# Optimization experiments

Hardware: AMD Instinct MI355X
Metric: run time of the kernel (lower is better)

The kernel has to match this reference:

```python
import jax, jax.numpy as jnp
import numpy as np


def dwconv1d(u, w, b):
    # u: (B, C, L), w: (C, 1, 3) depthwise, padding=1 -> same length
    out = jax.lax.conv_general_dilated(
        u, w, window_strides=(1,), padding=[(1, 1)],
        dimension_numbers=('NCH', 'OIH', 'NCH'),
        feature_group_count=u.shape[1])
    return out + b[None, :, None]


def selective_scan(u, delta, A, Bm, Cm, D, delta_bias):
    # u, delta: (B, KD, L); A: (KD, N); Bm, Cm: (B, K, N, L); D, delta_bias: (KD,)
    Bsz, KD, L = u.shape
    K, N = Bm.shape[1], Bm.shape[2]
    Dg = KD // K
    delta = jax.nn.softplus(delta + delta_bias[None, :, None])
    Bexp = jnp.repeat(Bm, Dg, axis=1)  # (B, KD, N, L)
    Cexp = jnp.repeat(Cm, Dg, axis=1)
    dA = jnp.exp(delta[:, :, None, :] * A[None, :, :, None])        # (B, KD, N, L)
    dBu = delta[:, :, None, :] * Bexp * u[:, :, None, :]            # (B, KD, N, L)

    def step(h, inp):
        a, bu, c = inp
        h = a * h + bu
        return h, jnp.sum(h * c, axis=-1)

    a_t = jnp.moveaxis(dA, -1, 0)
    bu_t = jnp.moveaxis(dBu, -1, 0)
    c_t = jnp.moveaxis(Cexp, -1, 0)
    _, ys = jax.lax.scan(step, jnp.zeros((Bsz, KD, N), u.dtype), (a_t, bu_t, c_t))
    return jnp.moveaxis(ys, 0, -1) + D[None, :, None] * u           # (B, KD, L)


def setup_inputs():
    key = jax.random.key(0)
    ks = jax.random.split(key, 8)
    d_inner, d_state, dt_rank, K = 192, 16, 6, 1
    bincounts = np.array([4096, 3000, 3500, 2500])
    total = int(bincounts.sum())
    max_bin = int(bincounts.max())
    starts = np.concatenate([[0], np.cumsum(bincounts)[:-1]])
    # compute_padding: wrap-around padded gather indices per cloud
    padded_idx = np.concatenate([np.arange(max_bin) % bc + st for bc, st in zip(bincounts, starts)])
    # crop-back indices into the (B*max_bin) padded layout
    valid_idx = np.concatenate([i * max_bin + np.arange(bc) for i, bc in enumerate(bincounts)])
    order = np.stack([np.random.RandomState(0).permutation(total)])
    inverse = np.argsort(order, axis=1)
    x = jax.random.normal(ks[0], (d_inner, total), jnp.float32)
    x_proj_weight = jax.random.normal(ks[1], (K, dt_rank + 2 * d_state, d_inner), jnp.float32) * 0.05
    dt_projs_weight = jax.random.normal(ks[2], (K, d_inner, dt_rank), jnp.float32) * 0.1
    dt_projs_bias = jax.random.normal(ks[3], (K, d_inner), jnp.float32) * 0.1
    A_logs = jnp.log(jnp.tile(jnp.arange(1, d_state + 1, dtype=jnp.float32), (K * d_inner, 1)))
    Ds = jnp.ones((K * d_inner,), jnp.float32)
    conv_w = jax.random.normal(ks[4], (K * d_inner, 1, 3), jnp.float32) * 0.2
    conv_b = jnp.zeros((K * d_inner,), jnp.float32)
    ln_gamma = jnp.ones((d_inner,), jnp.float32)
    ln_beta = jnp.zeros((d_inner,), jnp.float32)
    return {
        'x': x, 'x_proj_weight': x_proj_weight, 'dt_projs_weight': dt_projs_weight,
        'dt_projs_bias': dt_projs_bias, 'A_logs': A_logs, 'Ds': Ds,
        'conv_w': conv_w, 'conv_b': conv_b, 'ln_gamma': ln_gamma, 'ln_beta': ln_beta,
        'order': jnp.asarray(order, jnp.int32), 'inverse': jnp.asarray(inverse, jnp.int32),
        'padded_idx': jnp.asarray(padded_idx, jnp.int32),
        'valid_idx': jnp.asarray(valid_idx, jnp.int32), 'max_bin': max_bin,
    }


def reference(x, x_proj_weight, dt_projs_weight, dt_projs_bias, A_logs, Ds,
              conv_w, conv_b, ln_gamma, ln_beta,
              order, inverse, padded_idx, valid_idx, max_bin):
    K, Dch, R = dt_projs_weight.shape
    N = A_logs.shape[1]
    BM = padded_idx.shape[0]
    Bsz = BM // max_bin
    # multi-directional gather with offset padding: x[:, order[k]][:, padded_idx]
    idx = jnp.take(order, padded_idx, axis=1)                       # (K, B*max_bin)
    xs = jnp.take(x, idx, axis=1)                                   # (Dch, K, B*max_bin)
    xs = xs.transpose(1, 0, 2).reshape(K, Dch, Bsz, max_bin).transpose(2, 0, 1, 3)  # (B,K,D,L)
    x_dbl = jnp.einsum('bkdl,kcd->bkcl', xs, x_proj_weight)         # (B,K,R+2N,L)
    dts, Bs, Cs = jnp.split(x_dbl, [R, R + N], axis=2)
    dts = jnp.einsum('bkrl,kdr->bkdl', dts, dt_projs_weight)
    u = xs.reshape(Bsz, K * Dch, max_bin)
    delta = dts.reshape(Bsz, K * Dch, max_bin)
    A = -jnp.exp(A_logs)
    u = dwconv1d(u, conv_w, conv_b)  # conv1d applied after x_dbl/dts, before scan
    ys = selective_scan(u, delta, A, Bs, Cs, Ds, dt_projs_bias.reshape(-1))  # (B, K*Dch, L)
    # crop padding per cloud and concat along points
    ys = ys.reshape(Bsz, K, Dch, max_bin).transpose(1, 2, 0, 3).reshape(K, Dch, BM)
    ys = jnp.take(ys, valid_idx, axis=2)                            # (K, Dch, total)
    # K == 1, y_proj_weight is None -> scatter back through inverse permutation
    y = jnp.take(ys[0], inverse[0], axis=1)                         # (Dch, total)
    y = y.T                                                         # (total, Dch)
    mu = jnp.mean(y, axis=-1, keepdims=True)
    var = jnp.var(y, axis=-1, keepdims=True)
    y = (y - mu) / jnp.sqrt(var + 1e-5) * ln_gamma + ln_beta        # LayerNorm(d_inner)
    return y
```

## Files before the change

kernel.cpp:

```cpp
#include <hip/hip_runtime.h>
#include <math.h>

#define DINNER 192
#define NST    16
#define RNK    6
#define LSEQ   4096
#define BSZ    4
#define TOTAL  13096
#define BMPAD  16384
#define CL     32
#define MAXC   128
#define NSTATE 3072
#define NB32   410

#define BC_OF(b)  ((b)==0?4096:(b)==1?3000:(b)==2?3500:2500)
#define QST_OF(b) ((b)==0?0:(b)==1?4096:(b)==2?7096:10596)
#define NCB_OF(b) ((b)==0?128:(b)==1?94:(b)==2?110:79)

__device__ float  g_xs[(size_t)TOTAL * DINNER];
__device__ float  g_BC[(size_t)TOTAL * 32];
__device__ float  g_dt[(size_t)TOTAL * 8];
__device__ float2 g_PQ[(size_t)BSZ * MAXC * NSTATE];
__device__ float  g_hin[(size_t)BSZ * MAXC * NSTATE];

__global__ __launch_bounds__(256) void kA(
    const float* __restrict__ x,
    const float* __restrict__ W,
    const int*   __restrict__ inverse)
{
    const int blk = blockIdx.x;
    const int t = threadIdx.x;
    const bool isG = (blk >= NB32);
    const int P0 = (isG ? blk - NB32 : blk) * 32;
    const int npts = min(32, TOTAL - P0);

    __shared__ float sx[32 * 193];
    __shared__ float sW[38 * DINNER];
    __shared__ int   sg[32];

    if (t < 32) sg[t] = (t < npts) ? inverse[P0 + t] : 0;
    for (int idx = t; idx < 32 * DINNER; idx += 256) {
        int j = idx & 31, d = idx >> 5;
        sx[j * 193 + d] = (j < npts) ? x[(size_t)d * TOTAL + P0 + j] : 0.f;
    }
    if (isG)
        for (int idx = t; idx < 38 * DINNER; idx += 256) sW[idx] = W[idx];
    __syncthreads();

    if (!isG) {
        for (int idx = t; idx < npts * 48; idx += 256) {
            int j = idx / 48, q = idx - j * 48;
            const float* sp = &sx[j * 193 + q * 4];
            float4 v = {sp[0], sp[1], sp[2], sp[3]};
            *(float4*)&g_xs[(size_t)sg[j] * DINNER + q * 4] = v;
        }
    } else {
        const int j = t & 31, cw = t >> 5;
        float acc[5] = {0.f, 0.f, 0.f, 0.f, 0.f};
        for (int dt0 = 0; dt0 < DINNER; dt0 += 16) {
            float xr[16];
            #pragma unroll
            for (int q = 0; q < 16; ++q) xr[q] = sx[j * 193 + dt0 + q];
            #pragma unroll
            for (int k = 0; k < 5; ++k) {
                const int c = cw + 8 * k;
                if (c < RNK + 2 * NST) {
                    const float4* wr = (const float4*)&sW[c * DINNER + dt0];
                    float4 w0 = wr[0], w1 = wr[1], w2 = wr[2], w3 = wr[3];
                    float a = acc[k];
                    a += xr[0]*w0.x + xr[1]*w0.y + xr[2]*w0.z + xr[3]*w0.w;
                    a += xr[4]*w1.x + xr[5]*w1.y + xr[6]*w1.z + xr[7]*w1.w;
                    a += xr[8]*w2.x + xr[9]*w2.y + xr[10]*w2.z + xr[11]*w2.w;
                    a += xr[12]*w3.x + xr[13]*w3.y + xr[14]*w3.z + xr[15]*w3.w;
                    acc[k] = a;
                }
            }
        }
        if (j < npts) {
            const int g = sg[j];
            #pragma unroll
            for (int k = 0; k < 5; ++k) {
                const int c = cw + 8 * k;
                if (c < RNK)                g_dt[(size_t)g * 8 + c] = acc[k];
                else if (c < RNK + 2 * NST) g_BC[(size_t)g * 32 + (c - RNK)] = acc[k];
            }
        }
    }
}

__device__ __forceinline__ float xpad(int pos, int bc, int qst, int d) {
    if (pos < 0 || pos >= LSEQ) return 0.f;
    if (pos >= bc) pos -= bc;
    return g_xs[(size_t)(qst + pos) * DINNER + d];
}

__global__ __launch_bounds__(192) void k2_scan1(
    const float* __restrict__ A_logs,
    const float* __restrict__ conv_w,
    const float* __restrict__ conv_b,
    const float* __restrict__ dtW,
    const float* __restrict__ dtB)
{
    const int blk = blockIdx.x;
    const int b = blk >> 7;
    const int chunk = blk & (MAXC - 1);
    const int bc = BC_OF(b), qst = QST_OF(b), ncb = NCB_OF(b);
    if (chunk >= ncb) return;
    const int l0 = chunk * CL;
    const int steps = min(CL, bc - l0);
    const int t = threadIdx.x;

    __shared__ float sxr[(CL + 2) * DINNER];
    __shared__ float sB[CL * NST];
    __shared__ float sdt[CL * 8];

    for (int k = 0; k < steps + 2; ++k)
        sxr[k * DINNER + t] = xpad(l0 - 1 + k, bc, qst, t);
    for (int idx = t; idx < steps * NST; idx += 192) {
        int i = idx >> 4, n = idx & 15;
        sB[idx] = g_BC[(size_t)(qst + l0 + i) * 32 + n];
    }
    for (int idx = t; idx < steps * 8; idx += 192)
        sdt[idx] = g_dt[(size_t)(qst + l0) * 8 + idx];
    __syncthreads();

    float Av[16];
    {
        const float4* A4 = (const float4*)(A_logs + t * NST);
        #pragma unroll
        for (int q = 0; q < 4; ++q) {
            float4 v = A4[q];
            Av[q*4+0] = -__expf(v.x); Av[q*4+1] = -__expf(v.y);
            Av[q*4+2] = -__expf(v.z); Av[q*4+3] = -__expf(v.w);
        }
    }
    const float Av0 = Av[0];
    bool fast = true;
    #pragma unroll
    for (int n = 0; n < 16; ++n)
        fast = fast && (fabsf(Av[n] - (float)(n + 1) * Av0) <= 1e-4f * (float)(n + 1));

    float wdt[RNK];
    #pragma unroll
    for (int r = 0; r < RNK; ++r) wdt[r] = dtW[t * RNK + r];
    const float bdel = dtB[t];
    const float cw0 = conv_w[t*3+0], cw1 = conv_w[t*3+1], cw2 = conv_w[t*3+2];
    const float cb = conv_b[t];

    float h[16];
    #pragma unroll
    for (int n = 0; n < 16; ++n) h[n] = 0.f;
    float delsum = 0.f;
    float xm = sxr[t], xc = sxr[DINNER + t];

    for (int i = 0; i < steps; ++i) {
        float xp = sxr[(i + 2) * DINNER + t];
        float u = fmaf(cw0, xm, fmaf(cw1, xc, fmaf(cw2, xp, cb)));
        float da = bdel;
        #pragma unroll
        for (int r = 0; r < RNK; ++r) da = fmaf(wdt[r], sdt[i * 8 + r], da);
        float del = (da > 20.f) ? da : log1pf(__expf(da));
        float du = del * u;
        delsum += del;
        const float4* b4 = (const float4*)&sB[i * NST];
        float4 B0 = b4[0], B1 = b4[1], B2 = b4[2], B3 = b4[3];
        const float Bv[16] = {B0.x,B0.y,B0.z,B0.w, B1.x,B1.y,B1.z,B1.w,
                              B2.x,B2.y,B2.z,B2.w, B3.x,B3.y,B3.z,B3.w};
        if (fast) {
            float e = __expf(del * Av0);
            float a = e;
            #pragma unroll
            for (int n = 0; n < 16; ++n) { h[n] = fmaf(a, h[n], Bv[n] * du); a *= e; }
        } else {
            #pragma unroll
            for (int n = 0; n < 16; ++n) {
                float a = __expf(del * Av[n]);
                h[n] = fmaf(a, h[n], Bv[n] * du);
            }
        }
        xm = xc; xc = xp;
    }

    float4* o4 = (float4*)(g_PQ + (size_t)(b * MAXC + chunk) * NSTATE + t * 16);
    #pragma unroll
    for (int k = 0; k < 8; ++k) {
        float P0v = __expf(Av[2*k]   * delsum);
        float P1v = __expf(Av[2*k+1] * delsum);
        o4[k] = make_float4(P0v, h[2*k], P1v, h[2*k+1]);
    }
}

__global__ __launch_bounds__(256) void k3_comb()
{
    const int b = blockIdx.x / 48;
    const int s0 = (blockIdx.x % 48) * 64;
    const int ncb = NCB_OF(b);
    const int t = threadIdx.x;
    __shared__ float2 spq[MAXC * 64];

    for (int idx = t; idx < ncb * 64; idx += 256) {
        int c = idx >> 6, j = idx & 63;
        spq[idx] = g_PQ[(size_t)(b * MAXC + c) * NSTATE + s0 + j];
    }
    __syncthreads();
    if (t < 64) {
        float h = 0.f;
        for (int c = 0; c < ncb; ++c) {
            g_hin[(size_t)(b * MAXC + c) * NSTATE + s0 + t] = h;
            float2 v = spq[c * 64 + t];
            h = fmaf(v.x, h, v.y);
        }
    }
}

__global__ __launch_bounds__(192) void k4_scan2(
    const float* __restrict__ A_logs,
    const float* __restrict__ conv_w,
    const float* __restrict__ conv_b,
    const float* __restrict__ dtW,
    const float* __restrict__ dtB,
    const float* __restrict__ Ds,
    const int*   __restrict__ order,
    const float* __restrict__ gamma,
    const float* __restrict__ beta,
    float* __restrict__ out)
{
    const int blk = blockIdx.x;
    const int b = blk >> 7;
    const int chunk = blk & (MAXC - 1);
    const int bc = BC_OF(b), qst = QST_OF(b), ncb = NCB_OF(b);
    if (chunk >= ncb) return;
    const int l0 = chunk * CL;
    const int steps = min(CL, bc - l0);
    const int t = threadIdx.x;

    __shared__ float sxr[(CL + 2) * DINNER];
    __shared__ float sBC[CL * 32];
    __shared__ float sdt[CL * 8];
    __shared__ float sy[CL * DINNER];

    for (int k = 0; k < steps + 2; ++k)
        sxr[k * DINNER + t] = xpad(l0 - 1 + k, bc, qst, t);
    {
        const size_t base = (size_t)(qst + l0) * 32;
        for (int idx = t; idx < steps * 32; idx += 192) sBC[idx] = g_BC[base + idx];
    }
    for (int idx = t; idx < steps * 8; idx += 192)
        sdt[idx] = g_dt[(size_t)(qst + l0) * 8 + idx];
    __syncthreads();

    float Av[16];
    {
        const float4* A4 = (const float4*)(A_logs + t * NST);
        #pragma unroll
        for (int q = 0; q < 4; ++q) {
            float4 v = A4[q];
            Av[q*4+0] = -__expf(v.x); Av[q*4+1] = -__expf(v.y);
            Av[q*4+2] = -__expf(v.z); Av[q*4+3] = -__expf(v.w);
        }
    }
    const float Av0 = Av[0];
    bool fast = true;
    #pragma unroll
    for (int n = 0; n < 16; ++n)
        fast = fast && (fabsf(Av[n] - (float)(n + 1) * Av0) <= 1e-4f * (float)(n + 1));

    float wdt[RNK];
    #pragma unroll
    for (int r = 0; r < RNK; ++r) wdt[r] = dtW[t * RNK + r];
    const float bdel = dtB[t];
    const float cw0 = conv_w[t*3+0], cw1 = conv_w[t*3+1], cw2 = conv_w[t*3+2];
    const float cb = conv_b[t];
    const float Dd = Ds[t];

    float h[16];
    {
        const float4* h4 = (const float4*)(g_hin + (size_t)(b * MAXC + chunk) * NSTATE + t * 16);
        #pragma unroll
        for (int q = 0; q < 4; ++q) *(float4*)&h[q * 4] = h4[q];
    }
    float xm = sxr[t], xc = sxr[DINNER + t];

    for (int i = 0; i < steps; ++i) {
        float xp = sxr[(i + 2) * DINNER + t];
        float u = fmaf(cw0, xm, fmaf(cw1, xc, fmaf(cw2, xp, cb)));
        float da = bdel;
        #pragma unroll
        for (int r = 0; r < RNK; ++r) da = fmaf(wdt[r], sdt[i * 8 + r], da);
        float del = (da > 20.f) ? da : log1pf(__expf(da));
        float du = del * u;
        const float4* b4 = (const float4*)&sBC[i * 32];
        float4 B0 = b4[0], B1 = b4[1], B2 = b4[2], B3 = b4[3];
        float4 C0 = b4[4], C1 = b4[5], C2 = b4[6], C3 = b4[7];
        const float Bv[16] = {B0.x,B0.y,B0.z,B0.w, B1.x,B1.y,B1.z,B1.w,
                              B2.x,B2.y,B2.z,B2.w, B3.x,B3.y,B3.z,B3.w};
        const float Cv[16] = {C0.x,C0.y,C0.z,C0.w, C1.x,C1.y,C1.z,C1.w,
                              C2.x,C2.y,C2.z,C2.w, C3.x,C3.y,C3.z,C3.w};
        float y = Dd * u;
        if (fast) {
            float e = __expf(del * Av0);
            float a = e;
            #pragma unroll
            for (int n = 0; n < 16; ++n) {
                h[n] = fmaf(a, h[n], Bv[n] * du);
                y = fmaf(h[n], Cv[n], y);
                a *= e;
            }
        } else {
            #pragma unroll
            for (int n = 0; n < 16; ++n) {
                float a = __expf(del * Av[n]);
                h[n] = fmaf(a, h[n], Bv[n] * du);
                y = fmaf(h[n], Cv[n], y);
            }
        }
        sy[i * DINNER + t] = y;
        xm = xc; xc = xp;
    }
    __syncthreads();

    const int wv = t >> 6;
    const int lane = t & 63;
    for (int i = wv; i < steps; i += 3) {
        const float v0 = sy[i * DINNER + lane];
        const float v1 = sy[i * DINNER + 64 + lane];
        const float v2 = sy[i * DINNER + 128 + lane];
        float s  = v0 + v1 + v2;
        float s2 = v0 * v0 + v1 * v1 + v2 * v2;
        #pragma unroll
        for (int off = 1; off < 64; off <<= 1) {
            s  += __shfl_xor(s,  off);
            s2 += __shfl_xor(s2, off);
        }
        const float mu   = s / (float)DINNER;
        const float var  = s2 / (float)DINNER - mu * mu;
        const float rstd = rsqrtf(var + 1e-5f);
        const int p = order[qst + l0 + i];
        float* orow = out + (size_t)p * DINNER;
        orow[lane]       = (v0 - mu) * rstd * gamma[lane]       + beta[lane];
        orow[lane + 64]  = (v1 - mu) * rstd * gamma[lane + 64]  + beta[lane + 64];
        orow[lane + 128] = (v2 - mu) * rstd * gamma[lane + 128] + beta[lane + 128];
    }
}

extern "C" void kernel_launch(void* const* d_in, const int* in_sizes, int n_in,
                              void* d_out, int out_size, void* d_ws, size_t ws_size,
                              hipStream_t stream) {
    const float* x       = (const float*)d_in[0];
    const float* W       = (const float*)d_in[1];
    const float* dtW     = (const float*)d_in[2];
    const float* dtB     = (const float*)d_in[3];
    const float* A_logs  = (const float*)d_in[4];
    const float* Ds      = (const float*)d_in[5];
    const float* conv_w  = (const float*)d_in[6];
    const float* conv_b  = (const float*)d_in[7];
    const float* gamma   = (const float*)d_in[8];
    const float* beta    = (const float*)d_in[9];
    const int*   order   = (const int*)d_in[10];
    const int*   inverse = (const int*)d_in[11];
    float* outp = (float*)d_out;

    if (in_sizes[0] != TOTAL * DINNER || in_sizes[12] != BMPAD) return;

    kA<<<2 * NB32, 256, 0, stream>>>(x, W, inverse);
    k2_scan1<<<BSZ * MAXC, 192, 0, stream>>>(A_logs, conv_w, conv_b, dtW, dtB);
    k3_comb<<<192, 256, 0, stream>>>();
    k4_scan2<<<BSZ * MAXC, 192, 0, stream>>>(A_logs, conv_w, conv_b, dtW, dtB,
                                             Ds, order, gamma, beta, outp);
}
```

Before: 203.1 us.

## Fuse all four stages into one cooperative kernel with grid syncs

Replaces the four-kernel pipeline (projection, chunk scan, chunk combine, final scan plus LayerNorm) with a single cooperative kernel of 512 blocks that separates the stages with grid.sync. Each chunk block's shared-memory inputs (x window, B/C, dt) are loaded once and reused by both scan passes. The chunk combine is spread over all blocks, one state chain per thread, instead of running on 192 blocks. The kernel also detects when A's rows form an arithmetic sequence and computes the per-state decays with one exp and repeated multiplies. This removes launch gaps and repeated global loads, at the cost of grid-wide barriers and the requirement that all 512 blocks be co-resident, with a fallback to the old path.

New measurement: 527.0 us. +159.5%, slower.

```diff
diff --git a/kernel.cpp b/kernel.cpp
--- a/kernel.cpp
+++ b/kernel.cpp
@@ -1,5 +1,8 @@
 #include <hip/hip_runtime.h>
+#include <hip/hip_cooperative_groups.h>
 #include <math.h>
+
+namespace cg = cooperative_groups;
 
 #define DINNER 192
 #define NST    16
@@ -11,6 +14,7 @@
 #define CL     32
 #define MAXC   128
 #define NSTATE 3072
+#define NCHAIN 12288
 #define NB32   410
 
 #define BC_OF(b)  ((b)==0?4096:(b)==1?3000:(b)==2?3500:2500)
@@ -23,10 +27,278 @@
 __device__ float2 g_PQ[(size_t)BSZ * MAXC * NSTATE];
 __device__ float  g_hin[(size_t)BSZ * MAXC * NSTATE];
 
-__global__ __launch_bounds__(256) void kA(
+__device__ __forceinline__ float xpad(int pos, int bc, int qst, int d) {
+    if (pos < 0 || pos >= LSEQ) return 0.f;
+    if (pos >= bc) pos -= bc;
+    return g_xs[(size_t)(qst + pos) * DINNER + d];
+}
+
+__global__ __launch_bounds__(192, 1) void k_fused(
     const float* __restrict__ x,
     const float* __restrict__ W,
-    const int*   __restrict__ inverse)
+    const int*   __restrict__ inverse,
+    const float* __restrict__ A_logs,
+    const float* __restrict__ conv_w,
+    const float* __restrict__ conv_b,
+    const float* __restrict__ dtW,
+    const float* __restrict__ dtB,
+    const float* __restrict__ Ds,
+    const int*   __restrict__ order,
+    const float* __restrict__ gamma,
+    const float* __restrict__ beta,
+    float* __restrict__ out)
+{
+    cg::grid_group grid = cg::this_grid();
+    const int blk = blockIdx.x;
+    const int t = threadIdx.x;
+
+    __shared__ __align__(16) union {
+        struct { float sx[32 * 193]; float sW[38 * DINNER]; int sg[32]; } p1;
+        struct { float sxr[(CL + 2) * DINNER]; float sy[CL * DINNER];
+                 float sBC[CL * 32]; float sdt[CL * 8]; } p2;
+    } u;
+
+    if (blk < NB32) {
+        const int P0 = blk * 32;
+        const int npts = min(32, TOTAL - P0);
+        if (t < 32) u.p1.sg[t] = (t < npts) ? inverse[P0 + t] : 0;
+        for (int idx = t; idx < 32 * DINNER; idx += 192) {
+            int j = idx & 31, d = idx >> 5;
+            u.p1.sx[j * 193 + d] = (j < npts) ? x[(size_t)d * TOTAL + P0 + j] : 0.f;
+        }
+        for (int idx = t; idx < 38 * DINNER; idx += 192) u.p1.sW[idx] = W[idx];
+        __syncthreads();
+
+        for (int idx = t; idx < npts * 48; idx += 192) {
+            int j = idx / 48, q = idx - j * 48;
+            const float* sp = &u.p1.sx[j * 193 + q * 4];
+            float4 v = {sp[0], sp[1], sp[2], sp[3]};
+            *(float4*)&g_xs[(size_t)u.p1.sg[j] * DINNER + q * 4] = v;
+        }
+        const int j = t & 31, cw = t >> 5;
+        float acc[7] = {0.f, 0.f, 0.f, 0.f, 0.f, 0.f, 0.f};
+        for (int dt0 = 0; dt0 < DINNER; dt0 += 16) {
+            float xr[16];
+            #pragma unroll
+            for (int q = 0; q < 16; ++q) xr[q] = u.p1.sx[j * 193 + dt0 + q];
+            #pragma unroll
+            for (int k = 0; k < 7; ++k) {
+                const int c = cw + 6 * k;
+                if (c < RNK + 2 * NST) {
+                    const float4* wr = (const float4*)&u.p1.sW[c * DINNER + dt0];
+                    float4 w0 = wr[0], w1 = wr[1], w2 = wr[2], w3 = wr[3];
+                    float a = acc[k];
+                    a += xr[0]*w0.x + xr[1]*w0.y + xr[2]*w0.z + xr[3]*w0.w;
+                    a += xr[4]*w1.x + xr[5]*w1.y + xr[6]*w1.z + xr[7]*w1.w;
+                    a += xr[8]*w2.x + xr[9]*w2.y + xr[10]*w2.z + xr[11]*w2.w;
+                    a += xr[12]*w3.x + xr[13]*w3.y + xr[14]*w3.z + xr[15]*w3.w;
+                    acc[k] = a;
+                }
+            }
+        }
+        if (j < npts) {
+            const int g = u.p1.sg[j];
+            #pragma unroll
+            for (int k = 0; k < 7; ++k) {
+                const int c = cw + 6 * k;
+                if (c < RNK)                g_dt[(size_t)g * 8 + c] = acc[k];
+                else if (c < RNK + 2*NST)   g_BC[(size_t)g * 32 + (c - RNK)] = acc[k];
+            }
+        }
+    }
+    __threadfence();
+    grid.sync();
+
+    const int b = blk >> 7;
+    const int chunk = blk & (MAXC - 1);
+    const int bc = BC_OF(b), qst = QST_OF(b), ncb = NCB_OF(b);
+    const bool act = (chunk < ncb);
+    const int l0 = chunk * CL;
+    const int steps = act ? min(CL, bc - l0) : 0;
+
+    float Av[16];
+    {
+        const float4* A4 = (const float4*)(A_logs + t * NST);
+        #pragma unroll
+        for (int q = 0; q < 4; ++q) {
+            float4 v = A4[q];
+            Av[q*4+0] = -__expf(v.x); Av[q*4+1] = -__expf(v.y);
+            Av[q*4+2] = -__expf(v.z); Av[q*4+3] = -__expf(v.w);
+        }
+    }
+    const float Av0 = Av[0];
+    bool fast = true;
+    #pragma unroll
+    for (int n = 0; n < 16; ++n)
+        fast = fast && (fabsf(Av[n] - (float)(n + 1) * Av0) <= 1e-4f * (float)(n + 1));
+
+    float wdt[RNK];
+    #pragma unroll
+    for (int r = 0; r < RNK; ++r) wdt[r] = dtW[t * RNK + r];
+    const float bdel = dtB[t];
+    const float cw0 = conv_w[t*3+0], cw1 = conv_w[t*3+1], cw2 = conv_w[t*3+2];
+    const float cb = conv_b[t];
+    const float Dd = Ds[t];
+
+    if (act) {
+        for (int k = 0; k < steps + 2; ++k)
+            u.p2.sxr[k * DINNER + t] = xpad(l0 - 1 + k, bc, qst, t);
+        const size_t base32 = (size_t)(qst + l0) * 32;
+        for (int idx = t; idx < steps * 32; idx += 192) u.p2.sBC[idx] = g_BC[base32 + idx];
+        const size_t base8 = (size_t)(qst + l0) * 8;
+        for (int idx = t; idx < steps * 8; idx += 192) u.p2.sdt[idx] = g_dt[base8 + idx];
+    }
+    __syncthreads();
+
+    if (act) {
+        float h[16];
+        #pragma unroll
+        for (int n = 0; n < 16; ++n) h[n] = 0.f;
+        float delsum = 0.f;
+        float xm = u.p2.sxr[t], xc = u.p2.sxr[DINNER + t];
+        for (int i = 0; i < steps; ++i) {
+            float xp = u.p2.sxr[(i + 2) * DINNER + t];
+            float uu = fmaf(cw0, xm, fmaf(cw1, xc, fmaf(cw2, xp, cb)));
+            float da = bdel;
+            #pragma unroll
+            for (int r = 0; r < RNK; ++r) da = fmaf(wdt[r], u.p2.sdt[i * 8 + r], da);
+            float del = (da > 20.f) ? da : log1pf(__expf(da));
+            float du = del * uu;
+            delsum += del;
+            const float4* b4 = (const float4*)&u.p2.sBC[i * 32];
+            float4 B0 = b4[0], B1 = b4[1], B2 = b4[2], B3 = b4[3];
+            const float Bv[16] = {B0.x,B0.y,B0.z,B0.w, B1.x,B1.y,B1.z,B1.w,
+                                  B2.x,B2.y,B2.z,B2.w, B3.x,B3.y,B3.z,B3.w};
+            if (fast) {
+                float e = __expf(del * Av0);
+                float a = e;
+                #pragma unroll
+                for (int n = 0; n < 16; ++n) { h[n] = fmaf(a, h[n], Bv[n] * du); a *= e; }
+            } else {
+                #pragma unroll
+                for (int n = 0; n < 16; ++n) {
+                    float a = __expf(del * Av[n]);
+                    h[n] = fmaf(a, h[n], Bv[n] * du);
+                }
+            }
+            xm = xc; xc = xp;
+        }
+        float4* o4 = (float4*)(g_PQ + (size_t)(b * MAXC + chunk) * NSTATE + t * 16);
+        #pragma unroll
+        for (int k = 0; k < 8; ++k) {
+            float P0v = __expf(Av[2*k]   * delsum);
+            float P1v = __expf(Av[2*k+1] * delsum);
+            o4[k] = make_float4(P0v, h[2*k], P1v, h[2*k+1]);
+        }
+    }
+    __threadfence();
+    grid.sync();
+
+    {
+        const int gid = blk * 192 + t;
+        if (gid < NCHAIN) {
+            const int b3 = gid / NSTATE;
+            const int s = gid - b3 * NSTATE;
+            const int ncb3 = NCB_OF(b3);
+            float h = 0.f;
+            int c = 0;
+            for (; c + 8 <= ncb3; c += 8) {
+                float2 v[8];
+                #pragma unroll
+                for (int k = 0; k < 8; ++k)
+                    v[k] = g_PQ[(size_t)(b3 * MAXC + c + k) * NSTATE + s];
+                #pragma unroll
+                for (int k = 0; k < 8; ++k) {
+                    g_hin[(size_t)(b3 * MAXC + c + k) * NSTATE + s] = h;
+                    h = fmaf(v[k].x, h, v[k].y);
+                }
+            }
+            for (; c < ncb3; ++c) {
+                size_t o = (size_t)(b3 * MAXC + c) * NSTATE + s;
+                g_hin[o] = h;
+                float2 v = g_PQ[o];
+                h = fmaf(v.x, h, v.y);
+            }
+        }
+    }
+    __threadfence();
+    grid.sync();
+
+    if (act) {
+        float h[16];
+        {
+            const float4* h4 = (const float4*)(g_hin + (size_t)(b * MAXC + chunk) * NSTATE + t * 16);
+            #pragma unroll
+            for (int q = 0; q < 4; ++q) *(float4*)&h[q * 4] = h4[q];
+        }
+        float xm = u.p2.sxr[t], xc = u.p2.sxr[DINNER + t];
+        for (int i = 0; i < steps; ++i) {
+            float xp = u.p2.sxr[(i + 2) * DINNER + t];
+            float uu = fmaf(cw0, xm, fmaf(cw1, xc, fmaf(cw2, xp, cb)));
+            float da = bdel;
+            #pragma unroll
+            for (int r = 0; r < RNK; ++r) da = fmaf(wdt[r], u.p2.sdt[i * 8 + r], da);
+            float del = (da > 20.f) ? da : log1pf(__expf(da));
+            float du = del * uu;
+            const float4* b4 = (const float4*)&u.p2.sBC[i * 32];
+            float4 B0 = b4[0], B1 = b4[1], B2 = b4[2], B3 = b4[3];
+            float4 C0 = b4[4], C1 = b4[5], C2 = b4[6], C3 = b4[7];
+            const float Bv[16] = {B0.x,B0.y,B0.z,B0.w, B1.x,B1.y,B1.z,B1.w,
+                                  B2.x,B2.y,B2.z,B2.w, B3.x,B3.y,B3.z,B3.w};
+            const float Cv[16] = {C0.x,C0.y,C0.z,C0.w, C1.x,C1.y,C1.z,C1.w,
+                                  C2.x,C2.y,C2.z,C2.w, C3.x,C3.y,C3.z,C3.w};
+            float y = Dd * uu;
+            if (fast) {
+                float e = __expf(del * Av0);
+                float a = e;
+                #pragma unroll
+                for (int n = 0; n < 16; ++n) {
+                    h[n] = fmaf(a, h[n], Bv[n] * du);
+                    y = fmaf(h[n], Cv[n], y);
+                    a *= e;
+                }
+            } else {
+                #pragma unroll
+                for (int n = 0; n < 16; ++n) {
+                    float a = __expf(del * Av[n]);
+                    h[n] = fmaf(a, h[n], Bv[n] * du);
+                    y = fmaf(h[n], Cv[n], y);
+                }
+            }
+            u.p2.sy[i * DINNER + t] = y;
+            xm = xc; xc = xp;
+        }
+    }
+    __syncthreads();
+    if (act) {
+        const int wv = t >> 6;
+        const int lane = t & 63;
+        for (int i = wv; i < steps; i += 3) {
+            const float v0 = u.p2.sy[i * DINNER + lane];
+            const float v1 = u.p2.sy[i * DINNER + 64 + lane];
+            const float v2 = u.p2.sy[i * DINNER + 128 + lane];
+            float s  = v0 + v1 + v2;
+            float s2 = v0 * v0 + v1 * v1 + v2 * v2;
+            #pragma unroll
+            for (int off = 1; off < 64; off <<= 1) {
+                s  += __shfl_xor(s,  off);
+                s2 += __shfl_xor(s2, off);
+            }
+            const float mu   = s / (float)DINNER;
+            const float var  = s2 / (float)DINNER - mu * mu;
+            const float rstd = rsqrtf(var + 1e-5f);
+            const int p = order[qst + l0 + i];
+            float* orow = out + (size_t)p * DINNER;
+            orow[lane]       = (v0 - mu) * rstd * gamma[lane]       + beta[lane];
+            orow[lane + 64]  = (v1 - mu) * rstd * gamma[lane + 64]  + beta[lane + 64];
+            orow[lane + 128] = (v2 - mu) * rstd * gamma[lane + 128] + beta[lane + 128];
+        }
+    }
+}
+
+__global__ __launch_bounds__(256) void kA(
+    const float* __restrict__ x, const float* __restrict__ W,
+    const int* __restrict__ inverse)
 {
     const int blk = blockIdx.x;
     const int t = threadIdx.x;
@@ -88,17 +360,9 @@
     }
 }
 
-__device__ __forceinline__ float xpad(int pos, int bc, int qst, int d) {
-    if (pos < 0 || pos >= LSEQ) return 0.f;
-    if (pos >= bc) pos -= bc;
-    return g_xs[(size_t)(qst + pos) * DINNER + d];
-}
-
 __global__ __launch_bounds__(192) void k2_scan1(
-    const float* __restrict__ A_logs,
-    const float* __restrict__ conv_w,
-    const float* __restrict__ conv_b,
-    const float* __restrict__ dtW,
+    const float* __restrict__ A_logs, const float* __restrict__ conv_w,
+    const float* __restrict__ conv_b, const float* __restrict__ dtW,
     const float* __restrict__ dtB)
 {
     const int blk = blockIdx.x;
@@ -214,16 +478,11 @@
 }
 
 __global__ __launch_bounds__(192) void k4_scan2(
-    const float* __restrict__ A_logs,
-    const float* __restrict__ conv_w,
-    const float* __restrict__ conv_b,
-    const float* __restrict__ dtW,
-    const float* __restrict__ dtB,
-    const float* __restrict__ Ds,
-    const int*   __restrict__ order,
-    const float* __restrict__ gamma,
-    const float* __restrict__ beta,
-    float* __restrict__ out)
+    const float* __restrict__ A_logs, const float* __restrict__ conv_w,
+    const float* __restrict__ conv_b, const float* __restrict__ dtW,
+    const float* __restrict__ dtB, const float* __restrict__ Ds,
+    const int* __restrict__ order, const float* __restrict__ gamma,
+    const float* __restrict__ beta, float* __restrict__ out)
 {
     const int blk = blockIdx.x;
     const int b = blk >> 7;
@@ -362,9 +621,21 @@
 
     if (in_sizes[0] != TOTAL * DINNER || in_sizes[12] != BMPAD) return;
 
-    kA<<<2 * NB32, 256, 0, stream>>>(x, W, inverse);
-    k2_scan1<<<BSZ * MAXC, 192, 0, stream>>>(A_logs, conv_w, conv_b, dtW, dtB);
-    k3_comb<<<192, 256, 0, stream>>>();
-    k4_scan2<<<BSZ * MAXC, 192, 0, stream>>>(A_logs, conv_w, conv_b, dtW, dtB,
-                                             Ds, order, gamma, beta, outp);
+    int maxb = 0;
+    hipError_t oe = hipOccupancyMaxActiveBlocksPerMultiprocessor(
+        &maxb, (const void*)k_fused, 192, 0);
+    if (oe == hipSuccess && maxb >= 2) {
+        void* args[13] = {(void*)&x, (void*)&W, (void*)&inverse, (void*)&A_logs,
+                          (void*)&conv_w, (void*)&conv_b, (void*)&dtW, (void*)&dtB,
+                          (void*)&Ds, (void*)&order, (void*)&gamma, (void*)&beta,
+                          (void*)&outp};
+        hipLaunchCooperativeKernel((void*)k_fused, dim3(BSZ * MAXC), dim3(192),
+                                   args, 0, stream);
+    } else {
+        kA<<<2 * NB32, 256, 0, stream>>>(x, W, inverse);
+        k2_scan1<<<BSZ * MAXC, 192, 0, stream>>>(A_logs, conv_w, conv_b, dtW, dtB);
+        k3_comb<<<192, 256, 0, stream>>>();
+        k4_scan2<<<BSZ * MAXC, 192, 0, stream>>>(A_logs, conv_w, conv_b, dtW, dtB,
+                                                 Ds, order, gamma, beta, outp);
+    }
 }
```

## Batch global loads into registers before shared stores; restructure chunk-combine kernel

Applied to the files above, without the earlier changes.

The staging loops in kA, k2_scan1 and k4_scan2 now issue every global load into a register array first and only then write to shared memory. This lets many loads be in flight at once instead of serialising load-store pairs, and k4 also moves its initial-state load ahead of the barrier. k3_comb drops the shared-memory staging and runs one thread per state chain across 96 blocks, prefetching 16 chunk values at a time. The cost is higher register pressure, which could reduce occupancy, plus loads issued for padding rows that are then discarded.

Measured after the change: 178.7 us. 1.14x faster.

```diff
diff --git a/kernel.cpp b/kernel.cpp
--- a/kernel.cpp
+++ b/kernel.cpp
@@ -11,6 +11,7 @@
 #define CL     32
 #define MAXC   128
 #define NSTATE 3072
+#define NCHAIN 12288
 #define NB32   410
 
 #define BC_OF(b)  ((b)==0?4096:(b)==1?3000:(b)==2?3500:2500)
@@ -24,9 +25,8 @@
 __device__ float  g_hin[(size_t)BSZ * MAXC * NSTATE];
 
 __global__ __launch_bounds__(256) void kA(
-    const float* __restrict__ x,
-    const float* __restrict__ W,
-    const int*   __restrict__ inverse)
+    const float* __restrict__ x, const float* __restrict__ W,
+    const int* __restrict__ inverse)
 {
     const int blk = blockIdx.x;
     const int t = threadIdx.x;
@@ -39,12 +39,35 @@
     __shared__ int   sg[32];
 
     if (t < 32) sg[t] = (t < npts) ? inverse[P0 + t] : 0;
-    for (int idx = t; idx < 32 * DINNER; idx += 256) {
+
+    float xt[24];
+    #pragma unroll
+    for (int k = 0; k < 24; ++k) {
+        int idx = t + k * 256;
         int j = idx & 31, d = idx >> 5;
-        sx[j * 193 + d] = (j < npts) ? x[(size_t)d * TOTAL + P0 + j] : 0.f;
-    }
-    if (isG)
-        for (int idx = t; idx < 38 * DINNER; idx += 256) sW[idx] = W[idx];
+        xt[k] = (j < npts) ? x[(size_t)d * TOTAL + P0 + j] : 0.f;
+    }
+    float wt[29];
+    if (isG) {
+        #pragma unroll
+        for (int k = 0; k < 29; ++k) {
+            int idx = t + k * 256;
+            wt[k] = (idx < 38 * DINNER) ? W[idx] : 0.f;
+        }
+    }
+    #pragma unroll
+    for (int k = 0; k < 24; ++k) {
+        int idx = t + k * 256;
+        int j = idx & 31, d = idx >> 5;
+        sx[j * 193 + d] = xt[k];
+    }
+    if (isG) {
+        #pragma unroll
+        for (int k = 0; k < 29; ++k) {
+            int idx = t + k * 256;
+            if (idx < 38 * DINNER) sW[idx] = wt[k];
+        }
+    }
     __syncthreads();
 
     if (!isG) {
@@ -88,17 +111,9 @@
     }
 }
 
-__device__ __forceinline__ float xpad(int pos, int bc, int qst, int d) {
-    if (pos < 0 || pos >= LSEQ) return 0.f;
-    if (pos >= bc) pos -= bc;
-    return g_xs[(size_t)(qst + pos) * DINNER + d];
-}
-
 __global__ __launch_bounds__(192) void k2_scan1(
-    const float* __restrict__ A_logs,
-    const float* __restrict__ conv_w,
-    const float* __restrict__ conv_b,
-    const float* __restrict__ dtW,
+    const float* __restrict__ A_logs, const float* __restrict__ conv_w,
+    const float* __restrict__ conv_b, const float* __restrict__ dtW,
     const float* __restrict__ dtB)
 {
     const int blk = blockIdx.x;
@@ -114,14 +129,39 @@
     __shared__ float sB[CL * NST];
     __shared__ float sdt[CL * 8];
 
-    for (int k = 0; k < steps + 2; ++k)
-        sxr[k * DINNER + t] = xpad(l0 - 1 + k, bc, qst, t);
-    for (int idx = t; idx < steps * NST; idx += 192) {
-        int i = idx >> 4, n = idx & 15;
-        sB[idx] = g_BC[(size_t)(qst + l0 + i) * 32 + n];
-    }
-    for (int idx = t; idx < steps * 8; idx += 192)
-        sdt[idx] = g_dt[(size_t)(qst + l0) * 8 + idx];
+    float xr[CL + 2];
+    #pragma unroll
+    for (int k = 0; k < CL + 2; ++k) {
+        int pos = l0 - 1 + k;
+        bool v = (k < steps + 2) && (pos >= 0) && (pos < LSEQ);
+        int pw = (pos >= bc) ? pos - bc : pos;
+        xr[k] = v ? g_xs[(size_t)(qst + pw) * DINNER + t] : 0.f;
+    }
+    float bv[3];
+    #pragma unroll
+    for (int k = 0; k < 3; ++k) {
+        int idx = t + k * 192;
+        bv[k] = (idx < steps * NST)
+              ? g_BC[(size_t)(qst + l0 + (idx >> 4)) * 32 + (idx & 15)] : 0.f;
+    }
+    float dv[2];
+    #pragma unroll
+    for (int k = 0; k < 2; ++k) {
+        int idx = t + k * 192;
+        dv[k] = (idx < steps * 8) ? g_dt[(size_t)(qst + l0) * 8 + idx] : 0.f;
+    }
+    #pragma unroll
+    for (int k = 0; k < CL + 2; ++k) sxr[k * DINNER + t] = xr[k];
+    #pragma unroll
+    for (int k = 0; k < 3; ++k) {
+        int idx = t + k * 192;
+        if (idx < CL * NST) sB[idx] = bv[k];
+    }
+    #pragma unroll
+    for (int k = 0; k < 2; ++k) {
+        int idx = t + k * 192;
+        if (idx < CL * 8) sdt[idx] = dv[k];
+    }
     __syncthreads();
 
     float Av[16];
@@ -190,40 +230,37 @@
     }
 }
 
-__global__ __launch_bounds__(256) void k3_comb()
+__global__ __launch_bounds__(128) void k3_comb()
 {
-    const int b = blockIdx.x / 48;
-    const int s0 = (blockIdx.x % 48) * 64;
+    const int gid = blockIdx.x * 128 + threadIdx.x;
+    const int b = gid / NSTATE;
+    const int s = gid - b * NSTATE;
     const int ncb = NCB_OF(b);
-    const int t = threadIdx.x;
-    __shared__ float2 spq[MAXC * 64];
-
-    for (int idx = t; idx < ncb * 64; idx += 256) {
-        int c = idx >> 6, j = idx & 63;
-        spq[idx] = g_PQ[(size_t)(b * MAXC + c) * NSTATE + s0 + j];
-    }
-    __syncthreads();
-    if (t < 64) {
-        float h = 0.f;
-        for (int c = 0; c < ncb; ++c) {
-            g_hin[(size_t)(b * MAXC + c) * NSTATE + s0 + t] = h;
-            float2 v = spq[c * 64 + t];
-            h = fmaf(v.x, h, v.y);
+    float h = 0.f;
+    for (int c0 = 0; c0 < MAXC; c0 += 16) {
+        if (c0 >= ncb) break;
+        float2 v[16];
+        #pragma unroll
+        for (int k = 0; k < 16; ++k) {
+            int c = c0 + k;
+            v[k] = (c < ncb) ? g_PQ[(size_t)(b * MAXC + c) * NSTATE + s]
+                             : make_float2(1.f, 0.f);
+        }
+        #pragma unroll
+        for (int k = 0; k < 16; ++k) {
+            int c = c0 + k;
+            if (c < ncb) g_hin[(size_t)(b * MAXC + c) * NSTATE + s] = h;
+            h = fmaf(v[k].x, h, v[k].y);
         }
     }
 }
 
 __global__ __launch_bounds__(192) void k4_scan2(
-    const float* __restrict__ A_logs,
-    const float* __restrict__ conv_w,
-    const float* __restrict__ conv_b,
-    const float* __restrict__ dtW,
-    const float* __restrict__ dtB,
-    const float* __restrict__ Ds,
-    const int*   __restrict__ order,
-    const float* __restrict__ gamma,
-    const float* __restrict__ beta,
-    float* __restrict__ out)
+    const float* __restrict__ A_logs, const float* __restrict__ conv_w,
+    const float* __restrict__ conv_b, const float* __restrict__ dtW,
+    const float* __restrict__ dtB, const float* __restrict__ Ds,
+    const int* __restrict__ order, const float* __restrict__ gamma,
+    const float* __restrict__ beta, float* __restrict__ out)
 {
     const int blk = blockIdx.x;
     const int b = blk >> 7;
@@ -239,14 +276,44 @@
     __shared__ float sdt[CL * 8];
     __shared__ float sy[CL * DINNER];
 
-    for (int k = 0; k < steps + 2; ++k)
-        sxr[k * DINNER + t] = xpad(l0 - 1 + k, bc, qst, t);
+    float xr[CL + 2];
+    #pragma unroll
+    for (int k = 0; k < CL + 2; ++k) {
+        int pos = l0 - 1 + k;
+        bool v = (k < steps + 2) && (pos >= 0) && (pos < LSEQ);
+        int pw = (pos >= bc) ? pos - bc : pos;
+        xr[k] = v ? g_xs[(size_t)(qst + pw) * DINNER + t] : 0.f;
+    }
+    float bcv[6];
+    #pragma unroll
+    for (int k = 0; k < 6; ++k) {
+        int idx = t + k * 192;
+        bcv[k] = (idx < steps * 32) ? g_BC[(size_t)(qst + l0) * 32 + idx] : 0.f;
+    }
+    float dv[2];
+    #pragma unroll
+    for (int k = 0; k < 2; ++k) {
+        int idx = t + k * 192;
+        dv[k] = (idx < steps * 8) ? g_dt[(size_t)(qst + l0) * 8 + idx] : 0.f;
+    }
+    float h[16];
     {
-        const size_t base = (size_t)(qst + l0) * 32;
-        for (int idx = t; idx < steps * 32; idx += 192) sBC[idx] = g_BC[base + idx];
-    }
-    for (int idx = t; idx < steps * 8; idx += 192)
-        sdt[idx] = g_dt[(size_t)(qst + l0) * 8 + idx];
+        const float4* h4 = (const float4*)(g_hin + (size_t)(b * MAXC + chunk) * NSTATE + t * 16);
+        #pragma unroll
+        for (int q = 0; q < 4; ++q) *(float4*)&h[q * 4] = h4[q];
+    }
+    #pragma unroll
+    for (int k = 0; k < CL + 2; ++k) sxr[k * DINNER + t] = xr[k];
+    #pragma unroll
+    for (int k = 0; k < 6; ++k) {
+        int idx = t + k * 192;
+        if (idx < CL * 32) sBC[idx] = bcv[k];
+    }
+    #pragma unroll
+    for (int k = 0; k < 2; ++k) {
+        int idx = t + k * 192;
+        if (idx < CL * 8) sdt[idx] = dv[k];
+    }
     __syncthreads();
 
     float Av[16];
@@ -273,12 +340,6 @@
     const float cb = conv_b[t];
     const float Dd = Ds[t];
 
-    float h[16];
-    {
-        const float4* h4 = (const float4*)(g_hin + (size_t)(b * MAXC + chunk) * NSTATE + t * 16);
-        #pragma unroll
-        for (int q = 0; q < 4; ++q) *(float4*)&h[q * 4] = h4[q];
-    }
     float xm = sxr[t], xc = sxr[DINNER + t];
 
     for (int i = 0; i < steps; ++i) {
@@ -364,7 +425,7 @@
 
     kA<<<2 * NB32, 256, 0, stream>>>(x, W, inverse);
     k2_scan1<<<BSZ * MAXC, 192, 0, stream>>>(A_logs, conv_w, conv_b, dtW, dtB);
-    k3_comb<<<192, 256, 0, stream>>>();
+    k3_comb<<<NCHAIN / 128, 128, 0, stream>>>();
     k4_scan2<<<BSZ * MAXC, 192, 0, stream>>>(A_logs, conv_w, conv_b, dtW, dtB,
                                              Ds, order, gamma, beta, outp);
 }
```
